# Optimization experiments

Hardware: AMD Instinct MI355X
Metric: run time of the kernel (lower is better)

## Reference

```python
import jax, jax.numpy as jnp
import numpy as np
from jax import lax

N_LAYERS = 8
D_MODEL = 256
D_STATE = 64
EXPAND = 2
D_CONV = 4
HEADDIM = 32
D_INNER = EXPAND * D_MODEL            # 512
NHEADS = D_INNER // HEADDIM           # 16
CONV_DIM = D_INNER + 2 * D_STATE      # 640
D_IN_PROJ = 2 * D_INNER + 2 * D_STATE + NHEADS  # 1168
CHUNK = 64
B, L = 4, 2048
EPS = 1e-5


def setup_inputs() -> dict:
    key = jax.random.key(0)
    ks = iter(jax.random.split(key, 64))
    def rn(shape, s=1.0):
        return s * jax.random.normal(next(ks), shape, jnp.float32)
    inp = {"x": rn((B, L, D_MODEL))}
    for pre in ("fw", "bw"):
        inp[pre + "_ln_w"] = jnp.ones((N_LAYERS, D_MODEL), jnp.float32)
        inp[pre + "_ln_b"] = jnp.zeros((N_LAYERS, D_MODEL), jnp.float32)
        inp[pre + "_win"] = rn((N_LAYERS, D_IN_PROJ, D_MODEL), 0.05)
        inp[pre + "_convw"] = rn((N_LAYERS, CONV_DIM, D_CONV), 0.2)
        inp[pre + "_convb"] = jnp.zeros((N_LAYERS, CONV_DIM), jnp.float32)
        # A in [1, nheads] as in mamba2 init -> A_log = log(A)
        inp[pre + "_alog"] = jnp.log(jnp.tile(jnp.arange(1, NHEADS + 1, dtype=jnp.float32), (N_LAYERS, 1)))
        inp[pre + "_dtb"] = rn((N_LAYERS, NHEADS), 0.5)
        inp[pre + "_D"] = jnp.ones((N_LAYERS, NHEADS), jnp.float32)
        inp[pre + "_nw"] = jnp.ones((N_LAYERS, D_INNER), jnp.float32)
        inp[pre + "_wout"] = rn((N_LAYERS, D_MODEL, D_INNER), 0.05)
    inp["fusion_w"] = rn((D_MODEL, 2 * D_MODEL), 0.05)
    return inp


def _layernorm(x, w, b):
    mu = jnp.mean(x, -1, keepdims=True)
    v = jnp.mean(jnp.square(x - mu), -1, keepdims=True)
    return (x - mu) * lax.rsqrt(v + EPS) * w + b


def _ssd(xh, dt, A, Bm, Cm):
    # xh: (B,L,H,P)  dt: (B,L,H)  A: (H,)  Bm/Cm: (B,L,N).  Chunked SSD, chunk=CHUNK.
    Bb, Lq, H, P = xh.shape
    N = Bm.shape[-1]
    K = Lq // CHUNK
    xh = xh.reshape(Bb, K, CHUNK, H, P)
    dt = dt.reshape(Bb, K, CHUNK, H)
    Bm = Bm.reshape(Bb, K, CHUNK, N)
    Cm = Cm.reshape(Bb, K, CHUNK, N)
    dtA = dt * A                               # (B,K,C,H)
    cs = jnp.cumsum(dtA, axis=2)               # inclusive cumsum within chunk
    cs_t = cs.transpose(0, 1, 3, 2)            # (B,K,H,C)
    mask = jnp.tril(jnp.ones((CHUNK, CHUNK), bool))
    Lmat = jnp.where(mask, jnp.exp(cs_t[..., :, None] - cs_t[..., None, :]), 0.0)  # (B,K,H,C,C)
    CB = jnp.einsum('bkin,bkjn->bkij', Cm, Bm)  # (B,K,C,C)
    dt_t = dt.transpose(0, 1, 3, 2)             # (B,K,H,C)
    att = CB[:, :, None, :, :] * Lmat * dt_t[:, :, :, None, :]  # (B,K,H,C,C)
    y = jnp.einsum('bkhij,bkjhp->bkihp', att, xh)
    # chunk-local end states and cross-chunk recurrence
    decay_end = jnp.exp(cs_t[..., -1:] - cs_t)   # (B,K,H,C)
    w = decay_end * dt_t
    states = jnp.einsum('bkhj,bkjhp,bkjn->bkhpn', w, xh, Bm)  # (B,K,H,P,N)
    g = jnp.exp(cs_t[..., -1])                   # (B,K,H): total chunk decay
    def step(S, inputs):
        g_k, st_k = inputs
        return g_k[..., None, None] * S + st_k, S
    S0 = jnp.zeros((Bb, H, P, N), xh.dtype)
    _, Sprev = lax.scan(step, S0, (g.transpose(1, 0, 2), states.transpose(1, 0, 2, 3, 4)))
    # Sprev: (K,B,H,P,N) state at start of each chunk
    y_inter = jnp.einsum('bkin,kbhpn->bkihp', Cm, Sprev) * jnp.exp(cs)[..., None]
    return (y + y_inter).reshape(Bb, Lq, H, P)


def _mamba2(x, Win, convw, convb, A_log, dt_bias, Dp, norm_w, Wout):
    Bb, Lq, _ = x.shape
    zxbcdt = jnp.einsum('bld,ed->ble', x, Win)    # (B,L,D_IN_PROJ)
    z = zxbcdt[..., :D_INNER]
    xBC = zxbcdt[..., D_INNER:D_INNER + CONV_DIM]
    dt_raw = zxbcdt[..., D_INNER + CONV_DIM:]     # (B,L,H)
    # causal depthwise conv1d + silu
    xp = jnp.pad(xBC, ((0, 0), (D_CONV - 1, 0), (0, 0)))
    windows = jnp.stack([xp[:, k:k + Lq] for k in range(D_CONV)], axis=-1)  # (B,L,C,K)
    xc = jax.nn.silu(jnp.einsum('blck,ck->blc', windows, convw) + convb)
    xs = xc[..., :D_INNER].reshape(Bb, Lq, NHEADS, HEADDIM)
    Bm = xc[..., D_INNER:D_INNER + D_STATE]
    Cm = xc[..., D_INNER + D_STATE:]
    dt = jax.nn.softplus(dt_raw + dt_bias)
    A = -jnp.exp(A_log)
    y = _ssd(xs, dt, A, Bm, Cm) + Dp[None, None, :, None] * xs
    y = y.reshape(Bb, Lq, D_INNER)
    # gated RMSNorm (norm_before_gate=False): gate then normalize
    y = y * jax.nn.silu(z)
    y = y * lax.rsqrt(jnp.mean(jnp.square(y), -1, keepdims=True) + EPS) * norm_w
    return jnp.einsum('ble,de->bld', y, Wout)


def _run_stack(x, p):
    ln_w, ln_b, win, convw, convb, alog, dtb, Dp, nw, wout = p
    h = x
    for i in range(N_LAYERS):
        h = h + _mamba2(_layernorm(h, ln_w[i], ln_b[i]), win[i], convw[i], convb[i],
                        alog[i], dtb[i], Dp[i], nw[i], wout[i])
    return h


def reference(x,
              fw_ln_w, fw_ln_b, fw_win, fw_convw, fw_convb, fw_alog, fw_dtb, fw_D, fw_nw, fw_wout,
              bw_ln_w, bw_ln_b, bw_win, bw_convw, bw_convb, bw_alog, bw_dtb, bw_D, bw_nw, bw_wout,
              fusion_w):
    fw = (fw_ln_w, fw_ln_b, fw_win, fw_convw, fw_convb, fw_alog, fw_dtb, fw_D, fw_nw, fw_wout)
    bw = (bw_ln_w, bw_ln_b, bw_win, bw_convw, bw_convb, bw_alog, bw_dtb, bw_D, bw_nw, bw_wout)
    h_fwd = _run_stack(x, fw)
    h_bwd = jnp.flip(_run_stack(jnp.flip(x, 1), bw), 1)
    h = jnp.concatenate([h_fwd, h_bwd], axis=-1)      # (B,L,2D)
    return jnp.einsum('ble,de->bld', h, fusion_w)
```

## Files before the change

kernel.cpp:

```cpp
#include <hip/hip_runtime.h>
#include <math.h>


namespace {

constexpr int kL = 2048;
constexpr int kDM = 256;
constexpr int kDI = 512;
constexpr int kNH = 16;
constexpr int kDS = 64;
constexpr int kCDIM = 640;
constexpr int kDPROJ = 1168;
constexpr int kCH = 64;
constexpr int kKC = 32;
constexpr int kBB = 8;
constexpr int kRowsD = 4 * kL;
constexpr int kRows = kBB * kL;

typedef __bf16 bf16x8 __attribute__((ext_vector_type(8)));
typedef float f32x4 __attribute__((ext_vector_type(4)));
typedef unsigned short ushort;

union U16x8 {
  int4 v;
  ushort u[8];
  bf16x8 b;
};

__device__ __forceinline__ ushort f2b(float x) {
  union { float f; unsigned u; } c;
  c.f = x;
  unsigned r = c.u + 0x7fffu + ((c.u >> 16) & 1u);
  return (ushort)(r >> 16);
}
__device__ __forceinline__ float b2f(ushort u) {
  union { unsigned u; float f; } c;
  c.u = ((unsigned)u) << 16;
  return c.f;
}

__device__ __forceinline__ void gl_lds16(const void* g, void* l) {
  __builtin_amdgcn_global_load_lds(
      (const __attribute__((address_space(1))) unsigned int*)g,
      (__attribute__((address_space(3))) unsigned int*)l, 16, 0, 0);
}

constexpr int kQwin = 8 * kDPROJ * kDM / 4;
constexpr int kQwout = 8 * kDM * kDI / 4;
constexpr int kQfus = kDM * kDI / 4;
constexpr int kQtot = 2 * kQwin + 2 * kQwout + kQfus;

__global__ __launch_bounds__(256) void f2b_all_kernel(
    const float* __restrict__ s0, const float* __restrict__ s1,
    const float* __restrict__ s2, const float* __restrict__ s3,
    const float* __restrict__ s4, ushort* __restrict__ dst) {
  int i = blockIdx.x * 256 + threadIdx.x;
  if (i >= kQtot) return;
  const float* src;
  int off;
  if (i < kQwin) { src = s0; off = i; }
  else if (i < 2 * kQwin) { src = s1; off = i - kQwin; }
  else if (i < 2 * kQwin + kQwout) { src = s2; off = i - 2 * kQwin; }
  else if (i < 2 * kQwin + 2 * kQwout) { src = s3; off = i - 2 * kQwin - kQwout; }
  else { src = s4; off = i - 2 * kQwin - 2 * kQwout; }
  float4 v = *(const float4*)&src[(size_t)off * 4];
  ushort4 o = {f2b(v.x), f2b(v.y), f2b(v.z), f2b(v.w)};
  *(ushort4*)&dst[(size_t)i * 4] = o;
}

__global__ __launch_bounds__(256) void init_h_kernel(const float* __restrict__ x,
                                                     float* __restrict__ h) {
  int idx = blockIdx.x * 256 + threadIdx.x;
  if (idx >= 4 * kL * kDM) return;
  int d = idx & (kDM - 1);
  int l = (idx >> 8) & (kL - 1);
  int b = idx >> 19;
  float v = x[idx];
  h[idx] = v;
  h[((size_t)((4 + b) * kL + (kL - 1 - l))) * kDM + d] = v;
}

__global__ __launch_bounds__(256) void ln_kernel(const float* __restrict__ h,
                                                 const float* __restrict__ w0,
                                                 const float* __restrict__ b0,
                                                 const float* __restrict__ w1,
                                                 const float* __restrict__ b1,
                                                 ushort* __restrict__ xn) {
  int t = threadIdx.x;
  int lane = t & 63;
  int row = blockIdx.x * 4 + (t >> 6);
  int dir = (row >= kRowsD) ? 1 : 0;
  const float* w = dir ? w1 : w0;
  const float* b = dir ? b1 : b0;
  int e0 = lane * 4;
  float4 v = *(const float4*)&h[(size_t)row * kDM + e0];
  float s = v.x + v.y + v.z + v.w;
#pragma unroll
  for (int o = 32; o > 0; o >>= 1) s += __shfl_xor(s, o);
  float mu = s * (1.0f / kDM);
  float4 d = {v.x - mu, v.y - mu, v.z - mu, v.w - mu};
  float ss = d.x * d.x + d.y * d.y + d.z * d.z + d.w * d.w;
#pragma unroll
  for (int o = 32; o > 0; o >>= 1) ss += __shfl_xor(ss, o);
  float r = rsqrtf(ss * (1.0f / kDM) + 1e-5f);
  float4 wv = *(const float4*)&w[e0];
  float4 bv = *(const float4*)&b[e0];
  ushort4 o = {f2b(d.x * r * wv.x + bv.x), f2b(d.y * r * wv.y + bv.y),
               f2b(d.z * r * wv.z + bv.z), f2b(d.w * r * wv.w + bv.w)};
  *(ushort4*)&xn[(size_t)row * kDM + e0] = o;
}

__global__ __launch_bounds__(256) void gemm_bf16(const ushort* __restrict__ A,
                                                 const ushort* __restrict__ W0,
                                                 const ushort* __restrict__ W1,
                                                 ushort* __restrict__ C16,
                                                 float* __restrict__ dtraw, int Md,
                                                 int N, int K, int NT) {
  int dir = blockIdx.z;
  const ushort* W = dir ? W1 : W0;
  const ushort* Ab = A + (size_t)dir * Md * K;
  int wg = blockIdx.x;
  int chunk = gridDim.x >> 3;
  int swz = (wg & 7) * chunk + (wg >> 3);
  int m0 = (swz / NT) * 128;
  int n0 = (swz % NT) * 128;
  __shared__ __align__(16) ushort As[2][128 * 32];
  __shared__ __align__(16) ushort Ws[2][128 * 32];
  int tid = threadIdx.x;
  int lane = tid & 63;
  int wv = tid >> 6;
  int wr = (wv >> 1) * 64, wc = (wv & 1) * 64;
  int l16 = lane & 15, lk = lane >> 4;
  int rA = tid >> 2;
  int cA = (tid & 3) * 8;
  int rb0 = n0 + rA;       if (rb0 >= N) rb0 = N - 1;
  int rb1 = n0 + rA + 64;  if (rb1 >= N) rb1 = N - 1;

  f32x4 acc[4][4];
#pragma unroll
  for (int m = 0; m < 4; m++)
#pragma unroll
    for (int n = 0; n < 4; n++) acc[m][n] = {0.f, 0.f, 0.f, 0.f};

  for (int k0 = 0; k0 < K; k0 += 64) {
#pragma unroll
    for (int hh = 0; hh < 2; hh++) {
      int kk = k0 + hh * 32;
      gl_lds16(Ab + (size_t)(m0 + rA) * K + kk + cA, (char*)As[hh] + wv * 1024);
      gl_lds16(Ab + (size_t)(m0 + rA + 64) * K + kk + cA,
               (char*)As[hh] + 4096 + wv * 1024);
      gl_lds16(W + (size_t)rb0 * K + kk + cA, (char*)Ws[hh] + wv * 1024);
      gl_lds16(W + (size_t)rb1 * K + kk + cA, (char*)Ws[hh] + 4096 + wv * 1024);
    }
    __syncthreads();
#pragma unroll
    for (int hh = 0; hh < 2; hh++) {
      bf16x8 a[4], b[4];
#pragma unroll
      for (int m = 0; m < 4; m++)
        a[m] = *(const bf16x8*)((const char*)As[hh] +
                                (((wr + m * 16 + l16) * 32 + lk * 8) << 1));
#pragma unroll
      for (int n = 0; n < 4; n++)
        b[n] = *(const bf16x8*)((const char*)Ws[hh] +
                                (((wc + n * 16 + l16) * 32 + lk * 8) << 1));
#pragma unroll
      for (int m = 0; m < 4; m++)
#pragma unroll
        for (int n = 0; n < 4; n++)
          acc[m][n] =
              __builtin_amdgcn_mfma_f32_16x16x32_bf16(a[m], b[n], acc[m][n], 0, 0, 0);
    }
    __syncthreads();
  }
  ushort* Cb = C16 + (size_t)dir * Md * N;
  float* dtb = dtraw + (size_t)dir * Md * kNH;
#pragma unroll
  for (int m = 0; m < 4; m++) {
#pragma unroll
    for (int n = 0; n < 4; n++) {
      int col = n0 + wc + n * 16 + l16;
      if (col < N) {
#pragma unroll
        for (int r = 0; r < 4; r++) {
          int row = m0 + wr + m * 16 + lk * 4 + r;
          float v = acc[m][n][r];
          Cb[(size_t)row * N + col] = f2b(v);
          if (col >= 2 * kDI + 2 * kDS)
            dtb[(size_t)row * kNH + (col - (2 * kDI + 2 * kDS))] = v;
        }
      }
    }
  }
}

__global__ __launch_bounds__(256) void gemm_bf16_64(const ushort* __restrict__ A,
                                                    const ushort* __restrict__ W0,
                                                    const ushort* __restrict__ W1,
                                                    float* __restrict__ C, int Md,
                                                    int N, int K, int NT,
                                                    int accumulate) {
  int dir = blockIdx.z;
  const ushort* W = dir ? W1 : W0;
  const ushort* Ab = A + (size_t)dir * Md * K;
  float* Cb = C + (size_t)dir * Md * N;
  int wg = blockIdx.x;
  int chunk = gridDim.x >> 3;
  int swz = (wg & 7) * chunk + (wg >> 3);
  int m0 = (swz / NT) * 64;
  int n0 = (swz % NT) * 64;
  __shared__ __align__(16) ushort As[2][64 * 32];
  __shared__ __align__(16) ushort Ws[2][64 * 32];
  int tid = threadIdx.x;
  int lane = tid & 63;
  int wv = tid >> 6;
  int wr = (wv >> 1) * 32, wc = (wv & 1) * 32;
  int l16 = lane & 15, lk = lane >> 4;
  int rA = tid >> 2;
  int cA = (tid & 3) * 8;

  f32x4 acc[2][2];
#pragma unroll
  for (int m = 0; m < 2; m++)
#pragma unroll
    for (int n = 0; n < 2; n++) acc[m][n] = {0.f, 0.f, 0.f, 0.f};

  for (int k0 = 0; k0 < K; k0 += 64) {
#pragma unroll
    for (int hh = 0; hh < 2; hh++) {
      int kk = k0 + hh * 32;
      gl_lds16(Ab + (size_t)(m0 + rA) * K + kk + cA, (char*)As[hh] + wv * 1024);
      gl_lds16(W + (size_t)(n0 + rA) * K + kk + cA, (char*)Ws[hh] + wv * 1024);
    }
    __syncthreads();
#pragma unroll
    for (int hh = 0; hh < 2; hh++) {
      bf16x8 a[2], b[2];
#pragma unroll
      for (int m = 0; m < 2; m++)
        a[m] = *(const bf16x8*)((const char*)As[hh] +
                                (((wr + m * 16 + l16) * 32 + lk * 8) << 1));
#pragma unroll
      for (int n = 0; n < 2; n++)
        b[n] = *(const bf16x8*)((const char*)Ws[hh] +
                                (((wc + n * 16 + l16) * 32 + lk * 8) << 1));
#pragma unroll
      for (int m = 0; m < 2; m++)
#pragma unroll
        for (int n = 0; n < 2; n++)
          acc[m][n] =
              __builtin_amdgcn_mfma_f32_16x16x32_bf16(a[m], b[n], acc[m][n], 0, 0, 0);
    }
    __syncthreads();
  }
#pragma unroll
  for (int m = 0; m < 2; m++) {
#pragma unroll
    for (int n = 0; n < 2; n++) {
      int col = n0 + wc + n * 16 + l16;
#pragma unroll
      for (int r = 0; r < 4; r++) {
        int row = m0 + wr + m * 16 + lk * 4 + r;
        size_t idx = (size_t)row * N + col;
        float v = acc[m][n][r];
        if (accumulate) Cb[idx] += v;
        else Cb[idx] = v;
      }
    }
  }
}

constexpr int kConvBlocks = (kRows / 16) * (kCDIM / 8) / 256;

__global__ __launch_bounds__(256) void conv_cumsum_kernel(
    const ushort* __restrict__ zxb, const float* __restrict__ cw0,
    const float* __restrict__ cb0, const float* __restrict__ cw1,
    const float* __restrict__ cb1, ushort* __restrict__ xcb,
    const float* __restrict__ dtraw, const float* __restrict__ db0,
    const float* __restrict__ db1, const float* __restrict__ al0,
    const float* __restrict__ al1, float* __restrict__ dt,
    float* __restrict__ cs, float* __restrict__ g) {
  if ((int)blockIdx.x < kConvBlocks) {
    constexpr int kCG = kCDIM / 8;
    int idx = blockIdx.x * 256 + threadIdx.x;
    int c8 = (idx % kCG) * 8;
    int rt = idx / kCG;
    int bb = rt >> 7;
    int l0 = (rt & 127) << 4;
    int dir = bb >> 2;
    const float* cw = dir ? cw1 : cw0;
    const float* cb = dir ? cb1 : cb0;
    float wt[8][4];
#pragma unroll
    for (int c = 0; c < 8; c++) {
      float4 w = *(const float4*)&cw[(c8 + c) * 4];
      wt[c][0] = w.x; wt[c][1] = w.y; wt[c][2] = w.z; wt[c][3] = w.w;
    }
    float bias[8];
    {
      float4 b0 = *(const float4*)&cb[c8];
      float4 b1 = *(const float4*)&cb[c8 + 4];
      bias[0] = b0.x; bias[1] = b0.y; bias[2] = b0.z; bias[3] = b0.w;
      bias[4] = b1.x; bias[5] = b1.y; bias[6] = b1.z; bias[7] = b1.w;
    }
    const ushort* base = zxb + ((size_t)(bb * kL)) * kDPROJ + kDI + c8;
    float w0[8], w1[8], w2[8];
    if (l0 == 0) {
#pragma unroll
      for (int c = 0; c < 8; c++) { w0[c] = 0.f; w1[c] = 0.f; w2[c] = 0.f; }
    } else {
      U16x8 a, b, c;
      a.v = *(const int4*)(base + (size_t)(l0 - 3) * kDPROJ);
      b.v = *(const int4*)(base + (size_t)(l0 - 2) * kDPROJ);
      c.v = *(const int4*)(base + (size_t)(l0 - 1) * kDPROJ);
#pragma unroll
      for (int q = 0; q < 8; q++) {
        w0[q] = b2f(a.u[q]); w1[q] = b2f(b.u[q]); w2[q] = b2f(c.u[q]);
      }
    }
    ushort* outp = xcb + (size_t)(bb * kL + l0) * kCDIM + c8;
#pragma unroll
    for (int r = 0; r < 16; r++) {
      U16x8 cu;
      cu.v = *(const int4*)(base + (size_t)(l0 + r) * kDPROJ);
      U16x8 o;
#pragma unroll
      for (int c = 0; c < 8; c++) {
        float cf = b2f(cu.u[c]);
        float a = bias[c] + wt[c][0] * w0[c] + wt[c][1] * w1[c] + wt[c][2] * w2[c] +
                  wt[c][3] * cf;
        o.u[c] = f2b(a / (1.f + __expf(-a)));
        w0[c] = w1[c];
        w1[c] = w2[c];
        w2[c] = cf;
      }
      *(int4*)(outp + (size_t)r * kCDIM) = o.v;
    }
  } else {
    int t = threadIdx.x;
    int c = t & 63;
    int wid = ((int)blockIdx.x - kConvBlocks) * 4 + (t >> 6);
    int h = wid & (kNH - 1);
    int k = (wid >> 4) & (kKC - 1);
    int bb = wid >> 9;
    int dir = bb >> 2;
    int row = bb * kL + k * kCH + c;
    float x = dtraw[(size_t)row * kNH + h] + (dir ? db1 : db0)[h];
    float dtv = (x > 20.f) ? x : log1pf(expf(x));
    dt[(size_t)row * kNH + h] = dtv;
    float A = -__expf((dir ? al1 : al0)[h]);
    float s = dtv * A;
#pragma unroll
    for (int off = 1; off < 64; off <<= 1) {
      float u = __shfl_up(s, off);
      if (c >= off) s += u;
    }
    cs[(size_t)wid * kCH + c] = s;
    if (c == 63) g[wid] = __expf(s);
  }
}

__global__ __launch_bounds__(256) void states_kernel(const ushort* __restrict__ xcb,
                                                     const float* __restrict__ dt,
                                                     const float* __restrict__ cs,
                                                     ushort* __restrict__ states) {
  int bid = blockIdx.x;
  int half = bid & 1;
  int bk = bid >> 1;
  int k = bk & (kKC - 1);
  int bb = bk >> 5;
  __shared__ __align__(16) ushort Bstage[64][72];
  __shared__ __align__(16) ushort Bt[64][72];
  __shared__ __align__(16) ushort Ap[4][32][72];
  __shared__ float w_s[8][64];
  int t = threadIdx.x;
  int lane = t & 63, wv = t >> 6;
  size_t rowbase = (size_t)(bb * kL + k * kCH);
  {
    int j = t >> 2, n0 = (t & 3) * 16;
    const ushort* src = xcb + (rowbase + j) * kCDIM + kDI + n0;
    *(int4*)&Bstage[j][n0] = *(const int4*)src;
    *(int4*)&Bstage[j][n0 + 8] = *(const int4*)(src + 8);
  }
#pragma unroll
  for (int i = 0; i < 2; i++) {
    int e = t + i * 256;
    int hl = e >> 6, c = e & 63;
    int h = half * 8 + hl;
    const float* csb = cs + ((size_t)bk * 16 + h) * kCH;
    w_s[hl][c] = __expf(csb[63] - csb[c]) * dt[(rowbase + c) * kNH + h];
  }
  __syncthreads();
#pragma unroll
  for (int i = 0; i < 16; i++) {
    int e = t + i * 256;
    int j = e & 63, n = e >> 6;
    Bt[n][j] = Bstage[j][n];
  }
  __syncthreads();
  int l15 = lane & 15, lk8 = (lane >> 4) * 8;
  for (int hg = 0; hg < 2; hg++) {
    int hl = hg * 4 + wv;
    int h = half * 8 + hl;
    float wl = w_s[hl][lane];
    const ushort* xrow = xcb + (rowbase + lane) * kCDIM + h * 32;
#pragma unroll
    for (int q4 = 0; q4 < 4; q4++) {
      U16x8 v;
      v.v = *(const int4*)(xrow + q4 * 8);
#pragma unroll
      for (int q = 0; q < 8; q++)
        Ap[wv][q4 * 8 + q][lane] = f2b(b2f(v.u[q]) * wl);
    }
#pragma unroll
    for (int pt = 0; pt < 2; pt++) {
#pragma unroll
      for (int nt = 0; nt < 4; nt++) {
        f32x4 acc = {0.f, 0.f, 0.f, 0.f};
#pragma unroll
        for (int kt = 0; kt < 2; kt++) {
          bf16x8 a = *(const bf16x8*)&Ap[wv][pt * 16 + l15][kt * 32 + lk8];
          bf16x8 b = *(const bf16x8*)&Bt[nt * 16 + l15][kt * 32 + lk8];
          acc = __builtin_amdgcn_mfma_f32_16x16x32_bf16(a, b, acc, 0, 0, 0);
        }
        size_t base = ((size_t)bk * 16 + h) * 2048;
#pragma unroll
        for (int r = 0; r < 4; r++) {
          int p = pt * 16 + (lane >> 4) * 4 + r;
          states[base + p * 64 + nt * 16 + l15] = f2b(acc[r]);
        }
      }
    }
  }
}

__global__ __launch_bounds__(256) void scan_kernel(const ushort* __restrict__ st,
                                                   const float* __restrict__ g,
                                                   ushort* __restrict__ spbf) {
  int idx = blockIdx.x * 256 + threadIdx.x;
  if (idx >= kBB * kNH * 512) return;
  int pn4 = (idx & 511) * 4;
  int h = (idx >> 9) & (kNH - 1);
  int bb = idx >> 13;
  size_t base = ((size_t)(bb * kKC) * kNH + h) * 2048 + pn4;
  size_t stride = (size_t)kNH * 2048;
  const float* gp = g + bb * kKC * kNH + h;
  float S[4] = {0.f, 0.f, 0.f, 0.f};
  ushort4 sv = *(const ushort4*)&st[base];
  float gk = gp[0];
  for (int k = 0; k < kKC; k++) {
    size_t off = base + (size_t)k * stride;
    ushort4 so = {f2b(S[0]), f2b(S[1]), f2b(S[2]), f2b(S[3])};
    *(ushort4*)&spbf[off] = so;
    ushort4 nxt;
    float gn = 0.f;
    if (k < kKC - 1) {
      nxt = *(const ushort4*)&st[off + stride];
      gn = gp[(k + 1) * kNH];
    }
    S[0] = gk * S[0] + b2f(sv.x);
    S[1] = gk * S[1] + b2f(sv.y);
    S[2] = gk * S[2] + b2f(sv.z);
    S[3] = gk * S[3] + b2f(sv.w);
    sv = nxt;
    gk = gn;
  }
}

__global__ __launch_bounds__(256) void y_kernel(const ushort* __restrict__ xcb,
                                                const float* __restrict__ dt,
                                                const float* __restrict__ cs,
                                                const ushort* __restrict__ spbf,
                                                const float* __restrict__ D0,
                                                const float* __restrict__ D1,
                                                ushort* __restrict__ y) {
  int bid = blockIdx.x;
  int hq = bid & 3;
  int bk = bid >> 2;
  int k = bk & (kKC - 1);
  int bb = bk >> 5;
  int dir = bb >> 2;
  __shared__ __align__(16) ushort Cls[64][72];
  __shared__ __align__(16) ushort Bls[64][72];
  __shared__ float CBT[64][67];
  __shared__ __align__(16) ushort xs_s[64][40];
  __shared__ __align__(16) ushort xsT[32][72];
  __shared__ __align__(16) ushort sp_s[32][72];
  __shared__ float cs_s[64], dt_s[64], ecs_s[64];
  int t = threadIdx.x, lane = t & 63, wv = t >> 6;
  int l15 = lane & 15, lk8 = (lane >> 4) * 8;
  size_t rowbase = (size_t)(bb * kL + k * kCH);
  {
    int j = t >> 2, n0 = (t & 3) * 16;
    const ushort* pB = xcb + (rowbase + j) * kCDIM + kDI;
    *(int4*)&Bls[j][n0] = *(const int4*)(pB + n0);
    *(int4*)&Bls[j][n0 + 8] = *(const int4*)(pB + n0 + 8);
    *(int4*)&Cls[j][n0] = *(const int4*)(pB + kDS + n0);
    *(int4*)&Cls[j][n0 + 8] = *(const int4*)(pB + kDS + n0 + 8);
  }
  __syncthreads();
  {
    int i0 = wv * 16;
#pragma unroll
    for (int jt = 0; jt < 4; jt++) {
      f32x4 acc = {0.f, 0.f, 0.f, 0.f};
#pragma unroll
      for (int kt = 0; kt < 2; kt++) {
        bf16x8 a = *(const bf16x8*)&Cls[i0 + l15][kt * 32 + lk8];
        bf16x8 b = *(const bf16x8*)&Bls[jt * 16 + l15][kt * 32 + lk8];
        acc = __builtin_amdgcn_mfma_f32_16x16x32_bf16(a, b, acc, 0, 0, 0);
      }
#pragma unroll
      for (int r = 0; r < 4; r++)
        CBT[jt * 16 + l15][i0 + (lane >> 4) * 4 + r] = acc[r];
    }
  }
  for (int hi = 0; hi < 4; hi++) {
    int h = hq * 4 + hi;
    int bkh = bk * 16 + h;
    float Dp = (dir ? D1 : D0)[h];
    __syncthreads();
    {
      int j = t >> 2, p0 = (t & 3) * 8;
      U16x8 v;
      v.v = *(const int4*)(xcb + (rowbase + j) * kCDIM + h * 32 + p0);
      *(int4*)&xs_s[j][p0] = v.v;
#pragma unroll
      for (int q = 0; q < 8; q++) xsT[p0 + q][j] = v.u[q];
      int4 s = *(const int4*)(spbf + (size_t)bkh * 2048 + t * 8);
      *(int4*)&sp_s[t >> 3][(t & 7) * 8] = s;
      if (t < 64) {
        float cv = cs[(size_t)bkh * kCH + t];
        cs_s[t] = cv;
        ecs_s[t] = __expf(cv);
        dt_s[t] = dt[(rowbase + t) * kNH + h];
      }
    }
    __syncthreads();
    int i0 = wv * 16;
    int ia = i0 + l15;
    float csi = cs_s[ia];
    U16x8 af[2];
#pragma unroll
    for (int kt = 0; kt < 2; kt++) {
#pragma unroll
      for (int q = 0; q < 8; q++) {
        int j = kt * 32 + lk8 + q;
        float v = 0.f;
        if (j <= ia) v = __expf(csi - cs_s[j]) * dt_s[j] * CBT[j][ia];
        af[kt].u[q] = f2b(v);
      }
    }
#pragma unroll
    for (int pt = 0; pt < 2; pt++) {
      f32x4 acc = {0.f, 0.f, 0.f, 0.f};
      f32x4 acc2 = {0.f, 0.f, 0.f, 0.f};
#pragma unroll
      for (int kt = 0; kt < 2; kt++) {
        bf16x8 bx = *(const bf16x8*)&xsT[pt * 16 + l15][kt * 32 + lk8];
        acc = __builtin_amdgcn_mfma_f32_16x16x32_bf16(af[kt].b, bx, acc, 0, 0, 0);
        bf16x8 ac = *(const bf16x8*)&Cls[i0 + l15][kt * 32 + lk8];
        bf16x8 bs = *(const bf16x8*)&sp_s[pt * 16 + l15][kt * 32 + lk8];
        acc2 = __builtin_amdgcn_mfma_f32_16x16x32_bf16(ac, bs, acc2, 0, 0, 0);
      }
#pragma unroll
      for (int r = 0; r < 4; r++) {
        int io = i0 + (lane >> 4) * 4 + r;
        int p = pt * 16 + l15;
        float xsv = b2f(xs_s[io][p]);
        float v = acc[r] + ecs_s[io] * acc2[r] + Dp * xsv;
        y[(rowbase + io) * kDI + h * 32 + p] = f2b(v);
      }
    }
  }
}

__global__ __launch_bounds__(256) void gate_norm_kernel(const ushort* __restrict__ zxb,
                                                        const float* __restrict__ nw0,
                                                        const float* __restrict__ nw1,
                                                        const ushort* __restrict__ y,
                                                        ushort* __restrict__ ybf) {
  int t = threadIdx.x;
  int lane = t & 63;
  int row = blockIdx.x * 4 + (t >> 6);
  int dir = (row >= kRowsD) ? 1 : 0;
  const float* nw = dir ? nw1 : nw0;
  int e0 = lane * 8;
  U16x8 zu, yu;
  zu.v = *(const int4*)(zxb + (size_t)row * kDPROJ + e0);
  yu.v = *(const int4*)(y + (size_t)row * kDI + e0);
  float v[8];
  float ss = 0.f;
#pragma unroll
  for (int q = 0; q < 8; q++) {
    float z = b2f(zu.u[q]);
    float gz = z / (1.f + __expf(-z));
    v[q] = b2f(yu.u[q]) * gz;
    ss += v[q] * v[q];
  }
#pragma unroll
  for (int o = 32; o > 0; o >>= 1) ss += __shfl_xor(ss, o);
  float scale = rsqrtf(ss * (1.0f / kDI) + 1e-5f);
  float4 n0 = *(const float4*)&nw[e0];
  float4 n1 = *(const float4*)&nw[e0 + 4];
  float na[8] = {n0.x, n0.y, n0.z, n0.w, n1.x, n1.y, n1.z, n1.w};
  U16x8 o;
#pragma unroll
  for (int q = 0; q < 8; q++) o.u[q] = f2b(v[q] * scale * na[q]);
  *(int4*)&ybf[(size_t)row * kDI + e0] = o.v;
}

__global__ __launch_bounds__(256) void concat_kernel(const float* __restrict__ h,
                                                     ushort* __restrict__ hcat) {
  int idx = blockIdx.x * 256 + threadIdx.x;
  if (idx >= 4 * kL * 2 * kDM) return;
  int e = idx & 511;
  int l = (idx >> 9) & (kL - 1);
  int b = idx >> 20;
  float v;
  if (e < kDM)
    v = h[((size_t)(b * kL + l)) * kDM + e];
  else
    v = h[((size_t)((4 + b) * kL + (kL - 1 - l))) * kDM + (e - kDM)];
  hcat[idx] = f2b(v);
}

}

extern "C" void kernel_launch(void* const* d_in, const int* in_sizes, int n_in,
                              void* d_out, int out_size, void* d_ws, size_t ws_size,
                              hipStream_t stream) {
  const float* x = (const float*)d_in[0];
  const float* fw_ln_w = (const float*)d_in[1];
  const float* fw_ln_b = (const float*)d_in[2];
  const float* fw_win = (const float*)d_in[3];
  const float* fw_convw = (const float*)d_in[4];
  const float* fw_convb = (const float*)d_in[5];
  const float* fw_alog = (const float*)d_in[6];
  const float* fw_dtb = (const float*)d_in[7];
  const float* fw_D = (const float*)d_in[8];
  const float* fw_nw = (const float*)d_in[9];
  const float* fw_wout = (const float*)d_in[10];
  const float* bw_ln_w = (const float*)d_in[11];
  const float* bw_ln_b = (const float*)d_in[12];
  const float* bw_win = (const float*)d_in[13];
  const float* bw_convw = (const float*)d_in[14];
  const float* bw_convb = (const float*)d_in[15];
  const float* bw_alog = (const float*)d_in[16];
  const float* bw_dtb = (const float*)d_in[17];
  const float* bw_D = (const float*)d_in[18];
  const float* bw_nw = (const float*)d_in[19];
  const float* bw_wout = (const float*)d_in[20];
  const float* fusion_w = (const float*)d_in[21];
  float* out = (float*)d_out;

  float* ws = (float*)d_ws;
  float* h = ws;
  float* dtraw = h + (size_t)kRows * kDM;
  float* dt = dtraw + (size_t)kRows * kNH;
  float* cs = dt + (size_t)kRows * kNH;
  float* g = cs + (size_t)kBB * kKC * kNH * kCH;
  ushort* zxb = (ushort*)(g + (size_t)kBB * kKC * kNH);
  ushort* xcb = zxb + (size_t)kRows * kDPROJ;
  ushort* states = xcb + (size_t)kRows * kCDIM;
  ushort* spbf = states + (size_t)kBB * kKC * kNH * 2048;
  ushort* ybuf = spbf + (size_t)kBB * kKC * kNH * 2048;
  ushort* xnbf = ybuf + (size_t)kRows * kDI;
  ushort* ybf = xnbf + (size_t)kRows * kDM;
  ushort* winbf = ybf + (size_t)kRows * kDI;
  ushort* woutbf = winbf + (size_t)2 * 8 * kDPROJ * kDM;
  ushort* fusbf = woutbf + (size_t)2 * 8 * kDM * kDI;
  ushort* hcatbf = xnbf;

  f2b_all_kernel<<<(kQtot + 255) / 256, 256, 0, stream>>>(fw_win, bw_win, fw_wout,
                                                          bw_wout, fusion_w, winbf);
  init_h_kernel<<<(4 * kL * kDM + 255) / 256, 256, 0, stream>>>(x, h);

  for (int i = 0; i < 8; i++) {
    const size_t oLN = (size_t)i * kDM;
    const size_t oCW = (size_t)i * kCDIM * 4;
    const size_t oCB = (size_t)i * kCDIM;
    const size_t oH = (size_t)i * kNH;
    const size_t oNW = (size_t)i * kDI;
    const ushort* win0 = winbf + (size_t)i * kDPROJ * kDM;
    const ushort* win1 = winbf + (size_t)(8 + i) * kDPROJ * kDM;
    const ushort* wout0 = woutbf + (size_t)i * kDM * kDI;
    const ushort* wout1 = woutbf + (size_t)(8 + i) * kDM * kDI;

    ln_kernel<<<kRows / 4, 256, 0, stream>>>(h, fw_ln_w + oLN, fw_ln_b + oLN,
                                             bw_ln_w + oLN, bw_ln_b + oLN, xnbf);
    {
      dim3 grid(10 * 64, 1, 2);
      gemm_bf16<<<grid, 256, 0, stream>>>(xnbf, win0, win1, zxb, dtraw, kRowsD,
                                          kDPROJ, kDM, 10);
    }
    {
      int cumsumBlocks = kBB * kKC * kNH / 4;
      conv_cumsum_kernel<<<kConvBlocks + cumsumBlocks, 256, 0, stream>>>(
          zxb, fw_convw + oCW, fw_convb + oCB, bw_convw + oCW, bw_convb + oCB, xcb,
          dtraw, fw_dtb + oH, bw_dtb + oH, fw_alog + oH, bw_alog + oH, dt, cs, g);
    }
    states_kernel<<<kBB * kKC * 2, 256, 0, stream>>>(xcb, dt, cs, states);
    scan_kernel<<<(kBB * kNH * 512 + 255) / 256, 256, 0, stream>>>(states, g, spbf);
    y_kernel<<<kBB * kKC * 4, 256, 0, stream>>>(xcb, dt, cs, spbf, fw_D + oH,
                                                bw_D + oH, ybuf);
    gate_norm_kernel<<<kRows / 4, 256, 0, stream>>>(zxb, fw_nw + oNW, bw_nw + oNW,
                                                    ybuf, ybf);
    {
      dim3 grid(4 * 128, 1, 2);
      gemm_bf16_64<<<grid, 256, 0, stream>>>(ybf, wout0, wout1, h, kRowsD, kDM, kDI,
                                             4, 1);
    }
  }

  concat_kernel<<<(4 * kL * 2 * kDM + 255) / 256, 256, 0, stream>>>(h, hcatbf);
  {
    dim3 grid(4 * 128, 1, 1);
    gemm_bf16_64<<<grid, 256, 0, stream>>>(hcatbf, fusbf, fusbf, out, kRowsD, kDM,
                                           2 * kDM, 4, 0);
  }
}
```

Measured before the change: 947.8 us.

## Fuse gated RMSNorm into y kernel and out-projection GEMM epilogue

Removes the separate gate_norm kernel and its ybuf round trip. The y kernel now applies the SiLU gate itself, writes the gated bf16 output directly, and atomically accumulates each row's sum of squares into an rsum buffer, which the extra blocks added to the scan kernel zero beforehand. The norm weight is folded into the bf16 out-projection weights once at setup, and the GEMM epilogue scales each row by the reciprocal RMS. The cost is atomics and uncoalesced scalar z loads in the y kernel, and the normalization is now applied after bf16 rounding of the unnormalized values.

```diff
diff --git a/kernel.cpp b/kernel.cpp
--- a/kernel.cpp
+++ b/kernel.cpp
@@ -46,13 +46,11 @@
 }
 
 constexpr int kQwin = 8 * kDPROJ * kDM / 4;
-constexpr int kQwout = 8 * kDM * kDI / 4;
 constexpr int kQfus = kDM * kDI / 4;
-constexpr int kQtot = 2 * kQwin + 2 * kQwout + kQfus;
+constexpr int kQtot = 2 * kQwin + kQfus;
 
 __global__ __launch_bounds__(256) void f2b_all_kernel(
     const float* __restrict__ s0, const float* __restrict__ s1,
-    const float* __restrict__ s2, const float* __restrict__ s3,
     const float* __restrict__ s4, ushort* __restrict__ dst) {
   int i = blockIdx.x * 256 + threadIdx.x;
   if (i >= kQtot) return;
@@ -60,11 +58,31 @@
   int off;
   if (i < kQwin) { src = s0; off = i; }
   else if (i < 2 * kQwin) { src = s1; off = i - kQwin; }
-  else if (i < 2 * kQwin + kQwout) { src = s2; off = i - 2 * kQwin; }
-  else if (i < 2 * kQwin + 2 * kQwout) { src = s3; off = i - 2 * kQwin - kQwout; }
-  else { src = s4; off = i - 2 * kQwin - 2 * kQwout; }
+  else { src = s4; off = i - 2 * kQwin; }
   float4 v = *(const float4*)&src[(size_t)off * 4];
   ushort4 o = {f2b(v.x), f2b(v.y), f2b(v.z), f2b(v.w)};
+  *(ushort4*)&dst[(size_t)i * 4] = o;
+}
+
+constexpr int kQwoutAll = 2 * 8 * kDM * kDI / 4;
+
+__global__ __launch_bounds__(256) void wout_f2b_kernel(const float* __restrict__ fw,
+                                                       const float* __restrict__ bw,
+                                                       const float* __restrict__ fnw,
+                                                       const float* __restrict__ bnw,
+                                                       ushort* __restrict__ dst) {
+  int i = blockIdx.x * 256 + threadIdx.x;
+  if (i >= kQwoutAll) return;
+  int dl = i >> 15;
+  int rem = i & 32767;
+  int e4 = (rem & 127) * 4;
+  const float* src = (dl < 8) ? fw : bw;
+  const float* nw = (dl < 8) ? fnw : bnw;
+  int layer = dl & 7;
+  size_t so = (size_t)layer * kDM * kDI + (size_t)(rem >> 7) * kDI + e4;
+  float4 v = *(const float4*)&src[so];
+  float4 n = *(const float4*)&nw[layer * kDI + e4];
+  ushort4 o = {f2b(v.x * n.x), f2b(v.y * n.y), f2b(v.z * n.z), f2b(v.w * n.w)};
   *(ushort4*)&dst[(size_t)i * 4] = o;
 }
 
@@ -197,8 +215,9 @@
 __global__ __launch_bounds__(256) void gemm_bf16_64(const ushort* __restrict__ A,
                                                     const ushort* __restrict__ W0,
                                                     const ushort* __restrict__ W1,
-                                                    float* __restrict__ C, int Md,
-                                                    int N, int K, int NT,
+                                                    float* __restrict__ C,
+                                                    const float* __restrict__ rsum,
+                                                    int Md, int N, int K, int NT,
                                                     int accumulate) {
   int dir = blockIdx.z;
   const ushort* W = dir ? W1 : W0;
@@ -256,14 +275,17 @@
 #pragma unroll
   for (int m = 0; m < 2; m++) {
 #pragma unroll
-    for (int n = 0; n < 2; n++) {
-      int col = n0 + wc + n * 16 + l16;
-#pragma unroll
-      for (int r = 0; r < 4; r++) {
-        int row = m0 + wr + m * 16 + lk * 4 + r;
+    for (int r = 0; r < 4; r++) {
+      int row = m0 + wr + m * 16 + lk * 4 + r;
+      float sc = 1.f;
+      if (accumulate)
+        sc = rsqrtf(rsum[(size_t)dir * Md + row] * (1.0f / kDI) + 1e-5f);
+#pragma unroll
+      for (int n = 0; n < 2; n++) {
+        int col = n0 + wc + n * 16 + l16;
         size_t idx = (size_t)row * N + col;
         float v = acc[m][n][r];
-        if (accumulate) Cb[idx] += v;
+        if (accumulate) Cb[idx] += sc * v;
         else Cb[idx] = v;
       }
     }
@@ -436,9 +458,15 @@
 
 __global__ __launch_bounds__(256) void scan_kernel(const ushort* __restrict__ st,
                                                    const float* __restrict__ g,
-                                                   ushort* __restrict__ spbf) {
+                                                   ushort* __restrict__ spbf,
+                                                   float* __restrict__ rsum) {
+  if ((int)blockIdx.x >= 256) {
+    int i2 = ((int)blockIdx.x - 256) * 1024 + threadIdx.x * 4;
+    float4 z = {0.f, 0.f, 0.f, 0.f};
+    *(float4*)&rsum[i2] = z;
+    return;
+  }
   int idx = blockIdx.x * 256 + threadIdx.x;
-  if (idx >= kBB * kNH * 512) return;
   int pn4 = (idx & 511) * 4;
   int h = (idx >> 9) & (kNH - 1);
   int bb = idx >> 13;
@@ -468,12 +496,14 @@
 }
 
 __global__ __launch_bounds__(256) void y_kernel(const ushort* __restrict__ xcb,
+                                                const ushort* __restrict__ zxb,
                                                 const float* __restrict__ dt,
                                                 const float* __restrict__ cs,
                                                 const ushort* __restrict__ spbf,
                                                 const float* __restrict__ D0,
                                                 const float* __restrict__ D1,
-                                                ushort* __restrict__ y) {
+                                                float* __restrict__ rsum,
+                                                ushort* __restrict__ ybf) {
   int bid = blockIdx.x;
   int hq = bid & 3;
   int bk = bid >> 2;
@@ -515,6 +545,7 @@
         CBT[jt * 16 + l15][i0 + (lane >> 4) * 4 + r] = acc[r];
     }
   }
+  float ssr[4] = {0.f, 0.f, 0.f, 0.f};
   for (int hi = 0; hi < 4; hi++) {
     int h = hq * 4 + hi;
     int bkh = bk * 16 + h;
@@ -569,45 +600,27 @@
         int p = pt * 16 + l15;
         float xsv = b2f(xs_s[io][p]);
         float v = acc[r] + ecs_s[io] * acc2[r] + Dp * xsv;
-        y[(rowbase + io) * kDI + h * 32 + p] = f2b(v);
-      }
-    }
-  }
-}
-
-__global__ __launch_bounds__(256) void gate_norm_kernel(const ushort* __restrict__ zxb,
-                                                        const float* __restrict__ nw0,
-                                                        const float* __restrict__ nw1,
-                                                        const ushort* __restrict__ y,
-                                                        ushort* __restrict__ ybf) {
-  int t = threadIdx.x;
-  int lane = t & 63;
-  int row = blockIdx.x * 4 + (t >> 6);
-  int dir = (row >= kRowsD) ? 1 : 0;
-  const float* nw = dir ? nw1 : nw0;
-  int e0 = lane * 8;
-  U16x8 zu, yu;
-  zu.v = *(const int4*)(zxb + (size_t)row * kDPROJ + e0);
-  yu.v = *(const int4*)(y + (size_t)row * kDI + e0);
-  float v[8];
-  float ss = 0.f;
-#pragma unroll
-  for (int q = 0; q < 8; q++) {
-    float z = b2f(zu.u[q]);
-    float gz = z / (1.f + __expf(-z));
-    v[q] = b2f(yu.u[q]) * gz;
-    ss += v[q] * v[q];
-  }
-#pragma unroll
-  for (int o = 32; o > 0; o >>= 1) ss += __shfl_xor(ss, o);
-  float scale = rsqrtf(ss * (1.0f / kDI) + 1e-5f);
-  float4 n0 = *(const float4*)&nw[e0];
-  float4 n1 = *(const float4*)&nw[e0 + 4];
-  float na[8] = {n0.x, n0.y, n0.z, n0.w, n1.x, n1.y, n1.z, n1.w};
-  U16x8 o;
-#pragma unroll
-  for (int q = 0; q < 8; q++) o.u[q] = f2b(v[q] * scale * na[q]);
-  *(int4*)&ybf[(size_t)row * kDI + e0] = o.v;
+        float z = b2f(zxb[(rowbase + io) * kDPROJ + h * 32 + p]);
+        float gz = z / (1.f + __expf(-z));
+        float val = v * gz;
+        ybf[(rowbase + io) * kDI + h * 32 + p] = f2b(val);
+        ssr[r] += val * val;
+      }
+    }
+  }
+#pragma unroll
+  for (int o = 1; o < 16; o <<= 1) {
+#pragma unroll
+    for (int r = 0; r < 4; r++) ssr[r] += __shfl_xor(ssr[r], o);
+  }
+  if (l15 == 0) {
+    int i0 = wv * 16;
+#pragma unroll
+    for (int r = 0; r < 4; r++) {
+      int io = i0 + (lane >> 4) * 4 + r;
+      atomicAdd(&rsum[rowbase + io], ssr[r]);
+    }
+  }
 }
 
 __global__ __launch_bounds__(256) void concat_kernel(const float* __restrict__ h,
@@ -660,20 +673,22 @@
   float* dt = dtraw + (size_t)kRows * kNH;
   float* cs = dt + (size_t)kRows * kNH;
   float* g = cs + (size_t)kBB * kKC * kNH * kCH;
-  ushort* zxb = (ushort*)(g + (size_t)kBB * kKC * kNH);
+  float* rsum = g + (size_t)kBB * kKC * kNH;
+  ushort* zxb = (ushort*)(rsum + kRows);
   ushort* xcb = zxb + (size_t)kRows * kDPROJ;
   ushort* states = xcb + (size_t)kRows * kCDIM;
   ushort* spbf = states + (size_t)kBB * kKC * kNH * 2048;
-  ushort* ybuf = spbf + (size_t)kBB * kKC * kNH * 2048;
-  ushort* xnbf = ybuf + (size_t)kRows * kDI;
+  ushort* xnbf = spbf + (size_t)kBB * kKC * kNH * 2048;
   ushort* ybf = xnbf + (size_t)kRows * kDM;
   ushort* winbf = ybf + (size_t)kRows * kDI;
-  ushort* woutbf = winbf + (size_t)2 * 8 * kDPROJ * kDM;
-  ushort* fusbf = woutbf + (size_t)2 * 8 * kDM * kDI;
+  ushort* fusbf = winbf + (size_t)2 * 8 * kDPROJ * kDM;
+  ushort* woutbf = fusbf + (size_t)kDM * kDI;
   ushort* hcatbf = xnbf;
 
-  f2b_all_kernel<<<(kQtot + 255) / 256, 256, 0, stream>>>(fw_win, bw_win, fw_wout,
-                                                          bw_wout, fusion_w, winbf);
+  f2b_all_kernel<<<(kQtot + 255) / 256, 256, 0, stream>>>(fw_win, bw_win, fusion_w,
+                                                          winbf);
+  wout_f2b_kernel<<<(kQwoutAll + 255) / 256, 256, 0, stream>>>(fw_wout, bw_wout,
+                                                               fw_nw, bw_nw, woutbf);
   init_h_kernel<<<(4 * kL * kDM + 255) / 256, 256, 0, stream>>>(x, h);
 
   for (int i = 0; i < 8; i++) {
@@ -681,7 +696,6 @@
     const size_t oCW = (size_t)i * kCDIM * 4;
     const size_t oCB = (size_t)i * kCDIM;
     const size_t oH = (size_t)i * kNH;
-    const size_t oNW = (size_t)i * kDI;
     const ushort* win0 = winbf + (size_t)i * kDPROJ * kDM;
     const ushort* win1 = winbf + (size_t)(8 + i) * kDPROJ * kDM;
     const ushort* wout0 = woutbf + (size_t)i * kDM * kDI;
@@ -701,22 +715,20 @@
           dtraw, fw_dtb + oH, bw_dtb + oH, fw_alog + oH, bw_alog + oH, dt, cs, g);
     }
     states_kernel<<<kBB * kKC * 2, 256, 0, stream>>>(xcb, dt, cs, states);
-    scan_kernel<<<(kBB * kNH * 512 + 255) / 256, 256, 0, stream>>>(states, g, spbf);
-    y_kernel<<<kBB * kKC * 4, 256, 0, stream>>>(xcb, dt, cs, spbf, fw_D + oH,
-                                                bw_D + oH, ybuf);
-    gate_norm_kernel<<<kRows / 4, 256, 0, stream>>>(zxb, fw_nw + oNW, bw_nw + oNW,
-                                                    ybuf, ybf);
+    scan_kernel<<<256 + 16, 256, 0, stream>>>(states, g, spbf, rsum);
+    y_kernel<<<kBB * kKC * 4, 256, 0, stream>>>(xcb, zxb, dt, cs, spbf, fw_D + oH,
+                                                bw_D + oH, rsum, ybf);
     {
       dim3 grid(4 * 128, 1, 2);
-      gemm_bf16_64<<<grid, 256, 0, stream>>>(ybf, wout0, wout1, h, kRowsD, kDM, kDI,
-                                             4, 1);
+      gemm_bf16_64<<<grid, 256, 0, stream>>>(ybf, wout0, wout1, h, rsum, kRowsD,
+                                             kDM, kDI, 4, 1);
     }
   }
 
   concat_kernel<<<(4 * kL * 2 * kDM + 255) / 256, 256, 0, stream>>>(h, hcatbf);
   {
     dim3 grid(4 * 128, 1, 1);
-    gemm_bf16_64<<<grid, 256, 0, stream>>>(hcatbf, fusbf, fusbf, out, kRowsD, kDM,
-                                           2 * kDM, 4, 0);
-  }
-}
+    gemm_bf16_64<<<grid, 256, 0, stream>>>(hcatbf, fusbf, fusbf, out, nullptr,
+                                           kRowsD, kDM, 2 * kDM, 4, 0);
+  }
+}
```

Measured after the change: 911.1 us, median of 2. -3.9%, faster.
